# Optimization experiments

Hardware: AMD Instinct MI355X
Metric: run time of the kernel (lower is better)

Reference implementation:

```python
import jax, jax.numpy as jnp
import numpy as np

S, B, D, E2 = 2048, 32, 1024, 1024  # src_len, batch, dec_hid_dim, 2*enc_hid_dim


def setup_inputs() -> dict:
    key = jax.random.key(0)
    k1, k2, k3, k4, k5 = jax.random.split(key, 5)
    scale = 1.0 / np.sqrt(D)
    return {
        "dec_prev_hidden": jax.random.normal(k1, (B, D), dtype=jnp.float32),
        "enc_outputs": jax.random.normal(k2, (S, B, E2), dtype=jnp.float32),
        "Wb": jax.random.normal(k3, (D, D), dtype=jnp.float32) * scale,
        "Wc": jax.random.normal(k4, (D, E2), dtype=jnp.float32) * scale,
        "Wa": jax.random.normal(k5, (D,), dtype=jnp.float32) * scale,
    }


def reference(dec_prev_hidden, enc_outputs, Wb, Wc, Wa):
    # weighted_s_t_1: [B, D] broadcast over seq axis; weighted_H: [S, B, D]
    weighted_s = jnp.einsum('bd,ed->be', dec_prev_hidden, Wb)          # [B, D]
    weighted_H = jnp.einsum('sbe,de->sbd', enc_outputs, Wc)            # [S, B, D]
    score = jnp.einsum('sbd,d->sb', jnp.tanh(weighted_H + weighted_s), Wa)  # [S, B]
    # torch F.softmax with no dim on a 3-D tensor -> dim=0 (seq axis)
    attn = jax.nn.softmax(score, axis=0)                               # [S, B]
    # bmm([B,1,S], [B,S,2E]) -> [B,1,2E], then permute -> [1,B,2E]
    context = jnp.einsum('sb,sbe->be', attn, enc_outputs)              # [B, 2E]
    return context[None, :, :]                                         # [1, B, 2E]
```

## Files before the change

### kernel.cpp

```cpp
#include <hip/hip_runtime.h>
#include <hip/hip_bf16.h>
#include <stdint.h>

#define S_LEN 2048
#define BATCH 32
#define MROWS (S_LEN*BATCH)

typedef __attribute__((ext_vector_type(8))) short bf16x8;
typedef __attribute__((ext_vector_type(4))) float f32x4;
typedef unsigned short ushort_t;

__device__ inline unsigned int pk2bf(float a, float b) {
  float2 t; t.x = a; t.y = b;
  __hip_bfloat162 h = __float22bfloat162_rn(t);
  union { __hip_bfloat162 h; unsigned int u; } c; c.h = h;
  return c.u;
}

__device__ inline float bflo(unsigned int u) { return __uint_as_float(u << 16); }
__device__ inline float bfhi(unsigned int u) { return __uint_as_float(u & 0xffff0000u); }

__device__ inline void gload_lds16(const void* g, void* l) {
  __builtin_amdgcn_global_load_lds(
      (const __attribute__((address_space(1))) unsigned int*)g,
      (__attribute__((address_space(3))) unsigned int*)l, 16, 0, 0);
}

__device__ inline float fast_tanh(float x) {
  float e = __expf(2.0f * x);
  return 1.0f - 2.0f / (e + 1.0f);
}

__global__ __launch_bounds__(256) void prep_small_kernel(
    const float* __restrict__ dec, const float* __restrict__ Wb,
    const float* __restrict__ Wc, ushort_t* __restrict__ WcBf,
    float* __restrict__ wsum)
{
  const int t = threadIdx.x;
  const int bid = blockIdx.x;
  if (bid < 256) {
    const int base = bid * 4096;
    #pragma unroll
    for (int i = 0; i < 4; ++i) {
      int idx = base + i * 1024 + t * 4;
      float4 v = *(const float4*)(Wc + idx);
      uint2 w; w.x = pk2bf(v.x, v.y); w.y = pk2bf(v.z, v.w);
      *(uint2*)(WcBf + idx) = w;
    }
  } else {
    const int j = bid - 256;
    __shared__ float sdec[32][65];
    __shared__ float swb[32][65];
    const int b = t & 31, nl = t >> 5;
    float acc0 = 0.f, acc1 = 0.f, acc2 = 0.f, acc3 = 0.f;
    for (int c = 0; c < 16; ++c) {
      __syncthreads();
      for (int idx = t; idx < 2048; idx += 256) {
        int rr = idx >> 6, dd = idx & 63;
        sdec[rr][dd] = dec[rr * 1024 + c * 64 + dd];
        swb[rr][dd]  = Wb[(size_t)(j * 32 + rr) * 1024 + c * 64 + dd];
      }
      __syncthreads();
      #pragma unroll 8
      for (int dd = 0; dd < 64; ++dd) {
        float dv = sdec[b][dd];
        acc0 += dv * swb[nl][dd];
        acc1 += dv * swb[nl + 8][dd];
        acc2 += dv * swb[nl + 16][dd];
        acc3 += dv * swb[nl + 24][dd];
      }
    }
    wsum[b * 1024 + j * 32 + nl]      = acc0;
    wsum[b * 1024 + j * 32 + nl + 8]  = acc1;
    wsum[b * 1024 + j * 32 + nl + 16] = acc2;
    wsum[b * 1024 + j * 32 + nl + 24] = acc3;
  }
}

__global__ __launch_bounds__(256, 4) void score_kernel(
    const float4* __restrict__ encF4, ushort_t* __restrict__ encBf,
    const ushort_t* __restrict__ WcBf, const float* __restrict__ wsum,
    const float* __restrict__ Wa, float* __restrict__ scoreP8T)
{
  __shared__ ushort_t Ab[128][64];
  __shared__ ushort_t Bb[128][64];
  __shared__ float scorep[128];

  const int tid = threadIdx.x;
  const int lane = tid & 63;
  const int l15 = lane & 15, q = lane >> 4;
  const int r7 = l15 & 7;
  const int wid = tid >> 6;
  const int wr = wid >> 1, wc = wid & 1;
  const int bid = blockIdx.x;
  const int mi = bid & 15, nblk = (bid >> 4) & 7, mg = bid >> 7;
  const size_t rowBase = (size_t)(mg * 16 + mi) * 128;

  if (tid < 128) scorep[tid] = 0.f;

  const int tRow = tid >> 4;
  const int f4 = tid & 15;
  const int swzT = (((f4 >> 1) ^ (tRow & 7)) * 8) + ((f4 & 1) * 4);

  int bOff[4], dOff[4];
  #pragma unroll
  for (int k = 0; k < 4; ++k) {
    const int s = k * 256 + tid;
    const int r = s >> 3, c = s & 7;
    bOff[k] = (int)((nblk * 128 + r) * 1024 + ((c ^ (r & 7)) * 8));
    dOff[k] = s * 8;
  }
  ushort_t* const aL = &Ab[0][0];
  ushort_t* const bL = &Bb[0][0];

  int aRow[4], bRow[4];
  #pragma unroll
  for (int m = 0; m < 4; ++m) aRow[m] = (wr * 64 + m * 16 + l15) * 64;
  #pragma unroll
  for (int n = 0; n < 4; ++n) bRow[n] = (wc * 64 + n * 16 + l15) * 64;
  const int ch0 = (q ^ r7) * 8;
  const int ch1 = ((4 + q) ^ r7) * 8;

  f32x4 acc[4][4];
  #pragma unroll
  for (int m = 0; m < 4; ++m)
    #pragma unroll
    for (int n = 0; n < 4; ++n) { f32x4 z = {0.f,0.f,0.f,0.f}; acc[m][n] = z; }

  for (int kt = 0; kt < 16; ++kt) {
    const int ko = kt * 64;
    #pragma unroll
    for (int k = 0; k < 4; ++k)
      gload_lds16(WcBf + ko + bOff[k], bL + dOff[k]);

    float4 av[8];
    #pragma unroll
    for (int k = 0; k < 8; ++k)
      av[k] = encF4[(rowBase + k * 16 + tRow) * 256 + kt * 16 + f4];

    #pragma unroll
    for (int k = 0; k < 8; ++k) {
      uint2 w;
      w.x = pk2bf(av[k].x, av[k].y);
      w.y = pk2bf(av[k].z, av[k].w);
      const int r = k * 16 + tRow;
      *(uint2*)(aL + r * 64 + swzT) = w;
      if (nblk == 0)
        *(uint2*)(encBf + (rowBase + r) * 1024 + ko + f4 * 4) = w;
    }
    __syncthreads();

    #pragma unroll
    for (int kk = 0; kk < 2; ++kk) {
      const int cho = kk ? ch1 : ch0;
      bf16x8 af[4], bv[4];
      #pragma unroll
      for (int m = 0; m < 4; ++m) af[m] = *(const bf16x8*)(aL + aRow[m] + cho);
      #pragma unroll
      for (int n = 0; n < 4; ++n) bv[n] = *(const bf16x8*)(bL + bRow[n] + cho);
      #pragma unroll
      for (int m = 0; m < 4; ++m)
        #pragma unroll
        for (int n = 0; n < 4; ++n)
          acc[m][n] = __builtin_amdgcn_mfma_f32_16x16x32_bf16(
              af[m], bv[n], acc[m][n], 0, 0, 0);
    }
    __syncthreads();
  }

  #pragma unroll
  for (int m = 0; m < 4; ++m) {
    #pragma unroll
    for (int i = 0; i < 4; ++i) {
      const int rowl = wr * 64 + m * 16 + q * 4 + i;
      const int bb2 = rowl & 31;
      float v = 0.f;
      #pragma unroll
      for (int n = 0; n < 4; ++n) {
        const int col = nblk * 128 + wc * 64 + n * 16 + l15;
        float x = acc[m][n][i] + wsum[bb2 * 1024 + col];
        v += fast_tanh(x) * Wa[col];
      }
      v += __shfl_xor(v, 1); v += __shfl_xor(v, 2);
      v += __shfl_xor(v, 4); v += __shfl_xor(v, 8);
      if (l15 == 0) atomicAdd(&scorep[rowl], v);
    }
  }
  __syncthreads();
  if (tid < 128) {
    const int grow = (int)rowBase + tid;
    const int b = grow & 31, s = grow >> 5;
    scoreP8T[((b * 2048 + s) << 3) + nblk] = scorep[tid];
  }
}

__global__ __launch_bounds__(256) void ctx_partial_kernel(
    const ushort_t* __restrict__ encBf, const float* __restrict__ scoreP8T,
    float* __restrict__ partial, float* __restrict__ gSum)
{
  const int b = blockIdx.x & 31, sc = blockIdx.x >> 5;
  const int t = threadIdx.x;
  __shared__ float eCh[64];

  const int chunk0 = sc * 64;
  if (t < 64) {
    const float4* p = (const float4*)(scoreP8T +
                        (((size_t)b * 2048 + chunk0 + t) << 3));
    float4 u = p[0], v = p[1];
    float scv = ((u.x + u.y) + (u.z + u.w)) + ((v.x + v.y) + (v.z + v.w));
    float e = __expf(scv);
    eCh[t] = e;
    float sum = e;
    sum += __shfl_xor(sum, 1);  sum += __shfl_xor(sum, 2);
    sum += __shfl_xor(sum, 4);  sum += __shfl_xor(sum, 8);
    sum += __shfl_xor(sum, 16); sum += __shfl_xor(sum, 32);
    if (t == 0) gSum[sc * 32 + b] = sum;
  }
  __syncthreads();

  float a0 = 0.f, a1 = 0.f, a2 = 0.f, a3 = 0.f;
  const int e0 = t * 4;
  #pragma unroll 8
  for (int si = 0; si < 64; ++si) {
    const int s = chunk0 + si;
    const float a = eCh[si];
    uint2 w = *(const uint2*)(encBf + ((size_t)s * 32 + b) * 1024 + e0);
    a0 += a * bflo(w.x); a1 += a * bfhi(w.x);
    a2 += a * bflo(w.y); a3 += a * bfhi(w.y);
  }
  *(float4*)(partial + ((size_t)(sc * 32 + b)) * 1024 + e0) =
      make_float4(a0, a1, a2, a3);
}

__global__ __launch_bounds__(256) void ctx_reduce_kernel(
    const float* __restrict__ partial, const float* __restrict__ gSum,
    float* __restrict__ out)
{
  const int b = blockIdx.x, t = threadIdx.x;
  float tot = 0.f;
  #pragma unroll
  for (int sc = 0; sc < 32; ++sc) tot += gSum[sc * 32 + b];
  const float inv = 1.0f / tot;

  float4 acc = make_float4(0.f, 0.f, 0.f, 0.f);
  #pragma unroll
  for (int sc = 0; sc < 32; ++sc) {
    float4 v = *(const float4*)(partial + ((size_t)(sc * 32 + b)) * 1024 + t * 4);
    acc.x += v.x; acc.y += v.y; acc.z += v.z; acc.w += v.w;
  }
  acc.x *= inv; acc.y *= inv; acc.z *= inv; acc.w *= inv;
  *(float4*)(out + (size_t)b * 1024 + t * 4) = acc;
}

extern "C" void kernel_launch(void* const* d_in, const int* in_sizes, int n_in,
                              void* d_out, int out_size, void* d_ws, size_t ws_size,
                              hipStream_t stream) {
  const float* dec = (const float*)d_in[0];
  const float* enc = (const float*)d_in[1];
  const float* Wb  = (const float*)d_in[2];
  const float* Wc  = (const float*)d_in[3];
  const float* Wa  = (const float*)d_in[4];
  float* out = (float*)d_out;
  (void)in_sizes; (void)n_in; (void)ws_size; (void)out_size;

  char* ws = (char*)d_ws;
  ushort_t* encBf    = (ushort_t*)ws;
  ushort_t* WcBf     = (ushort_t*)(ws + 134217728);
  float*    wsum     = (float*)(ws + 134217728 + 2097152);
  float*    scoreP8T = (float*)(ws + 134217728 + 2097152 + 131072);
  float*    partial  = (float*)(ws + 134217728 + 2097152 + 131072 + 2097152);
  float*    gSum     = (float*)(ws + 134217728 + 2097152 + 131072 + 2097152 + 4194304);

  prep_small_kernel<<<288, 256, 0, stream>>>(dec, Wb, Wc, WcBf, wsum);
  score_kernel<<<4096, 256, 0, stream>>>((const float4*)enc, encBf, WcBf,
                                         wsum, Wa, scoreP8T);
  ctx_partial_kernel<<<1024, 256, 0, stream>>>(encBf, scoreP8T, partial, gSum);
  ctx_reduce_kernel<<<32, 256, 0, stream>>>(partial, gSum, out);
}
```

Before: 366.5 us.

## Split score GEMM: first two N-blocks read fp32, rest reuse bf16 copy

The score GEMM is split into two kernels. The first covers N-blocks 0-1, reading fp32 encoder outputs, converting them to bf16 and writing the bf16 copy. The second covers N-blocks 2-7 and loads the bf16 encoder copy straight into LDS with global_load_lds, so those blocks avoid repeated fp32 reads and conversions. The cost is an extra kernel launch and a serial dependency between the two launches.

```diff
diff --git a/kernel.cpp b/kernel.cpp
--- a/kernel.cpp
+++ b/kernel.cpp
@@ -77,7 +77,7 @@
   }
 }
 
-__global__ __launch_bounds__(256, 4) void score_kernel(
+__global__ __launch_bounds__(256, 4) void score_a_kernel(
     const float4* __restrict__ encF4, ushort_t* __restrict__ encBf,
     const ushort_t* __restrict__ WcBf, const float* __restrict__ wsum,
     const float* __restrict__ Wa, float* __restrict__ scoreP8T)
@@ -93,7 +93,8 @@
   const int wid = tid >> 6;
   const int wr = wid >> 1, wc = wid & 1;
   const int bid = blockIdx.x;
-  const int mi = bid & 15, nblk = (bid >> 4) & 7, mg = bid >> 7;
+  const int mi = bid & 15, nbi = (bid >> 4) & 1, mg = bid >> 5;
+  const int nblk = nbi;
   const size_t rowBase = (size_t)(mg * 16 + mi) * 128;
 
   if (tid < 128) scorep[tid] = 0.f;
@@ -145,8 +146,113 @@
       w.y = pk2bf(av[k].z, av[k].w);
       const int r = k * 16 + tRow;
       *(uint2*)(aL + r * 64 + swzT) = w;
-      if (nblk == 0)
+      if (nbi == 0)
         *(uint2*)(encBf + (rowBase + r) * 1024 + ko + f4 * 4) = w;
+    }
+    __syncthreads();
+
+    #pragma unroll
+    for (int kk = 0; kk < 2; ++kk) {
+      const int cho = kk ? ch1 : ch0;
+      bf16x8 af[4], bv[4];
+      #pragma unroll
+      for (int m = 0; m < 4; ++m) af[m] = *(const bf16x8*)(aL + aRow[m] + cho);
+      #pragma unroll
+      for (int n = 0; n < 4; ++n) bv[n] = *(const bf16x8*)(bL + bRow[n] + cho);
+      #pragma unroll
+      for (int m = 0; m < 4; ++m)
+        #pragma unroll
+        for (int n = 0; n < 4; ++n)
+          acc[m][n] = __builtin_amdgcn_mfma_f32_16x16x32_bf16(
+              af[m], bv[n], acc[m][n], 0, 0, 0);
+    }
+    __syncthreads();
+  }
+
+  #pragma unroll
+  for (int m = 0; m < 4; ++m) {
+    #pragma unroll
+    for (int i = 0; i < 4; ++i) {
+      const int rowl = wr * 64 + m * 16 + q * 4 + i;
+      const int bb2 = rowl & 31;
+      float v = 0.f;
+      #pragma unroll
+      for (int n = 0; n < 4; ++n) {
+        const int col = nblk * 128 + wc * 64 + n * 16 + l15;
+        float x = acc[m][n][i] + wsum[bb2 * 1024 + col];
+        v += fast_tanh(x) * Wa[col];
+      }
+      v += __shfl_xor(v, 1); v += __shfl_xor(v, 2);
+      v += __shfl_xor(v, 4); v += __shfl_xor(v, 8);
+      if (l15 == 0) atomicAdd(&scorep[rowl], v);
+    }
+  }
+  __syncthreads();
+  if (tid < 128) {
+    const int grow = (int)rowBase + tid;
+    const int b = grow & 31, s = grow >> 5;
+    scoreP8T[((b * 2048 + s) << 3) + nblk] = scorep[tid];
+  }
+}
+
+__global__ __launch_bounds__(256, 4) void score_b_kernel(
+    const ushort_t* __restrict__ encBf, const ushort_t* __restrict__ WcBf,
+    const float* __restrict__ wsum, const float* __restrict__ Wa,
+    float* __restrict__ scoreP8T)
+{
+  __shared__ ushort_t Ab[128][64];
+  __shared__ ushort_t Bb[128][64];
+  __shared__ float scorep[128];
+
+  const int tid = threadIdx.x;
+  const int lane = tid & 63;
+  const int l15 = lane & 15, q = lane >> 4;
+  const int r7 = l15 & 7;
+  const int wid = tid >> 6;
+  const int wr = wid >> 1, wc = wid & 1;
+  const int bid = blockIdx.x;
+  const int rem = bid % 96;
+  const int mi = rem & 15, nbi = rem >> 4;
+  const int nblk = nbi + 2;
+  const int mg = bid / 96;
+  const size_t rowBase = (size_t)(mg * 16 + mi) * 128;
+
+  if (tid < 128) scorep[tid] = 0.f;
+
+  int aOff[4], bOff[4], dOff[4];
+  #pragma unroll
+  for (int k = 0; k < 4; ++k) {
+    const int s = k * 256 + tid;
+    const int r = s >> 3, c = s & 7;
+    const int swz = (c ^ (r & 7)) * 8;
+    aOff[k] = (int)(r * 1024 + swz);
+    bOff[k] = (int)((nblk * 128 + r) * 1024 + swz);
+    dOff[k] = s * 8;
+  }
+  const ushort_t* aBase = encBf + rowBase * 1024;
+  ushort_t* const aL = &Ab[0][0];
+  ushort_t* const bL = &Bb[0][0];
+
+  int aRow[4], bRow[4];
+  #pragma unroll
+  for (int m = 0; m < 4; ++m) aRow[m] = (wr * 64 + m * 16 + l15) * 64;
+  #pragma unroll
+  for (int n = 0; n < 4; ++n) bRow[n] = (wc * 64 + n * 16 + l15) * 64;
+  const int ch0 = (q ^ r7) * 8;
+  const int ch1 = ((4 + q) ^ r7) * 8;
+
+  f32x4 acc[4][4];
+  #pragma unroll
+  for (int m = 0; m < 4; ++m)
+    #pragma unroll
+    for (int n = 0; n < 4; ++n) { f32x4 z = {0.f,0.f,0.f,0.f}; acc[m][n] = z; }
+
+  for (int kt = 0; kt < 16; ++kt) {
+    const int ko = kt * 64;
+    #pragma unroll
+    for (int k = 0; k < 4; ++k) {
+      gload_lds16(aBase + ko + aOff[k], aL + dOff[k]);
+      gload_lds16(WcBf + ko + bOff[k], bL + dOff[k]);
     }
     __syncthreads();
 
@@ -272,8 +378,9 @@
   float*    gSum     = (float*)(ws + 134217728 + 2097152 + 131072 + 2097152 + 4194304);
 
   prep_small_kernel<<<288, 256, 0, stream>>>(dec, Wb, Wc, WcBf, wsum);
-  score_kernel<<<4096, 256, 0, stream>>>((const float4*)enc, encBf, WcBf,
-                                         wsum, Wa, scoreP8T);
+  score_a_kernel<<<1024, 256, 0, stream>>>((const float4*)enc, encBf, WcBf,
+                                           wsum, Wa, scoreP8T);
+  score_b_kernel<<<3072, 256, 0, stream>>>(encBf, WcBf, wsum, Wa, scoreP8T);
   ctx_partial_kernel<<<1024, 256, 0, stream>>>(encBf, scoreP8T, partial, gSum);
   ctx_reduce_kernel<<<32, 256, 0, stream>>>(partial, gSum, out);
 }
```

Measured after the change: 372.0 us. No clear change (+1.5%).
